# Kernel optimization log

Measured on AMD Instinct MI355X. Metric: run time of the kernel, lower is better.

The kernel has to match this reference:

```python
import jax, jax.numpy as jnp
import numpy as np


def _mlp(x, W0, b0, W1, b1, W2, b2, W3, b3):
    # nlayers=4 MLP: 3->128->128->128->3 with ReLU between layers
    h = jax.nn.relu(x @ W0 + b0)
    h = jax.nn.relu(h @ W1 + b1)
    h = jax.nn.relu(h @ W2 + b2)
    return h @ W3 + b3


def setup_inputs() -> dict:
    key = jax.random.key(0)
    ks = jax.random.split(key, 8)
    B, Nc, Nt, Dx, Dy, H = 8, 1024, 1024, 3, 32, 128
    s = lambda fan: 1.0 / np.sqrt(fan)
    return {
        "xc": jax.random.normal(ks[0], (B, Nc, Dx), jnp.float32),
        "yc": jax.random.normal(ks[1], (B, Nc, Dy), jnp.float32),
        "xt": jax.random.normal(ks[2], (B, Nt, Dx), jnp.float32),
        "W0": jax.random.normal(ks[3], (Dx, H), jnp.float32) * s(Dx),
        "b0": jnp.zeros((H,), jnp.float32),
        "W1": jax.random.normal(ks[4], (H, H), jnp.float32) * s(H),
        "b1": jnp.zeros((H,), jnp.float32),
        "W2": jax.random.normal(ks[5], (H, H), jnp.float32) * s(H),
        "b2": jnp.zeros((H,), jnp.float32),
        "W3": jax.random.normal(ks[6], (H, Dx), jnp.float32) * s(H),
        "b3": jnp.zeros((Dx,), jnp.float32),
    }


def reference(xc, yc, xt, W0, b0, W1, b1, W2, b2, W3, b3):
    # sigmas: per-target, per-coordinate positive scales  (B, Nt, Dx)
    sig = jnp.exp(_mlp(xt, W0, b0, W1, b1, W2, b2, W3, b3))
    # squared differences (B, Nc, Nt, Dx), scaled and reduced over Dx
    A = (xc[:, :, None, :] - xt[:, None, :, :]) ** 2
    P = -(A * sig[:, None, :, :]).sum(axis=3)        # (B, Nc, Nt)
    S = jax.nn.softmax(P, axis=1)                    # softmax over context
    # weighted average of context values: (B, Nt, Dy)
    return jnp.einsum("bnd,bnt->btd", yc, S)
```

## Files before the change

### kernel.cpp

```cpp
#include <hip/hip_runtime.h>
#include <math.h>

#define BB 8
#define NCC 1024
#define NTT 1024
#define HH 128
#define DYY 32
#define NTB 16
#define LOG2E 1.44269504088896340736f

typedef _Float16 half8 __attribute__((ext_vector_type(8)));
typedef float f32x4 __attribute__((ext_vector_type(4)));

#define HB 0
#define RED 2112
#define XCW 2496
#define SIGL 5568
#define SMEM_SZ 5616
#define CMB 0
#define SL 4224
#define HSTRIDE 132

__global__ __launch_bounds__(512, 2) void k_fused(const float* __restrict__ xc,
                                                  const float* __restrict__ yc,
                                                  const float* __restrict__ xt,
                                                  const float* __restrict__ W0,
                                                  const float* __restrict__ b0,
                                                  const float* __restrict__ W1,
                                                  const float* __restrict__ b1,
                                                  const float* __restrict__ W2,
                                                  const float* __restrict__ b2,
                                                  const float* __restrict__ W3,
                                                  const float* __restrict__ b3,
                                                  float* __restrict__ out) {
    const int tid = threadIdx.x;
    const int phys = blockIdx.x;
    const int bid = (phys & 7) * 64 + (phys >> 3);
    const int t0 = bid * NTB;
    const int b = bid >> 6;
    const int wv = tid >> 6;
    const int lane = tid & 63;

    __shared__ float smem[SMEM_SZ];

    const float4* __restrict__ xcG4 = (const float4*)(xc + (size_t)b * NCC * 3);

    const int jg = tid >> 4;
    const int p = tid & 15;
    const int j0 = jg * 4;
    float* hrow = smem + HB + p * HSTRIDE;

    {
        const float* xr = xt + (size_t)(t0 + p) * 3;
        const float x0 = xr[0], x1 = xr[1], x2 = xr[2];
        const float4* W0v = (const float4*)W0;
        const float4 w0a = W0v[jg], w0b = W0v[32 + jg], w0c = W0v[64 + jg];
        const float4 bb0 = ((const float4*)b0)[jg];
        float4 h0;
        h0.x = fmaxf(fmaf(x0, w0a.x, fmaf(x1, w0b.x, fmaf(x2, w0c.x, bb0.x))), 0.f);
        h0.y = fmaxf(fmaf(x0, w0a.y, fmaf(x1, w0b.y, fmaf(x2, w0c.y, bb0.y))), 0.f);
        h0.z = fmaxf(fmaf(x0, w0a.z, fmaf(x1, w0b.z, fmaf(x2, w0c.z, bb0.z))), 0.f);
        h0.w = fmaxf(fmaf(x0, w0a.w, fmaf(x1, w0b.w, fmaf(x2, w0c.w, bb0.w))), 0.f);
        *(float4*)(hrow + j0) = h0;
    }

    {
        float* xcw = smem + XCW + wv * 384;
        if (lane < 48) {
            float4 tx0 = xcG4[wv * 96 + lane];
            float4 tx1 = xcG4[wv * 96 + 48 + lane];
            ((float4*)xcw)[lane] = tx0;
            ((float4*)xcw)[lane + 48] = tx1;
        }
    }
    __syncthreads();

    {
        const int mtl = lane & 15;
        const int mg = lane >> 4;
        const int jcol = wv * 16 + mtl;

#pragma unroll
        for (int l = 0; l < 2; ++l) {
            const float* __restrict__ Wg = (l == 0) ? W1 : W2;
            const float* __restrict__ bi = (l == 0) ? b1 : b2;
            f32x4 dac;
            {
                const float bj = bi[jcol];
                dac[0] = bj; dac[1] = bj; dac[2] = bj; dac[3] = bj;
            }
            float w[8];
#pragma unroll
            for (int i = 0; i < 8; ++i) w[i] = Wg[(mg * 8 + i) * HH + jcol];
#pragma unroll
            for (int c = 0; c < 4; ++c) {
                float wn[8];
                if (c < 3) {
#pragma unroll
                    for (int i = 0; i < 8; ++i)
                        wn[i] = Wg[((c + 1) * 32 + mg * 8 + i) * HH + jcol];
                }
                float hv[8];
                *(float4*)hv =
                    *(const float4*)(smem + HB + mtl * HSTRIDE + c * 32 + mg * 8);
                *(float4*)(hv + 4) =
                    *(const float4*)(smem + HB + mtl * HSTRIDE + c * 32 + mg * 8 + 4);
                half8 a0, a1, bf0, bf1;
#pragma unroll
                for (int i = 0; i < 8; ++i) {
                    const _Float16 ah = (_Float16)hv[i];
                    a0[i] = ah;
                    a1[i] = (_Float16)(hv[i] - (float)ah);
                    const _Float16 wh = (_Float16)w[i];
                    bf0[i] = wh;
                    bf1[i] = (_Float16)(w[i] - (float)wh);
                }
                dac = __builtin_amdgcn_mfma_f32_16x16x32_f16(a0, bf0, dac, 0, 0, 0);
                dac = __builtin_amdgcn_mfma_f32_16x16x32_f16(a0, bf1, dac, 0, 0, 0);
                dac = __builtin_amdgcn_mfma_f32_16x16x32_f16(a1, bf0, dac, 0, 0, 0);
                if (c < 3) {
#pragma unroll
                    for (int i = 0; i < 8; ++i) w[i] = wn[i];
                }
            }
            __syncthreads();
#pragma unroll
            for (int r = 0; r < 4; ++r)
                smem[HB + (mg * 4 + r) * HSTRIDE + jcol] = fmaxf(dac[r], 0.f);
            __syncthreads();
        }
    }

    {
        const float4 o4 = *(const float4*)(hrow + j0);
        const float4* W3v = (const float4*)W3;
        const float4 wr0 = W3v[jg * 3 + 0];
        const float4 wr1 = W3v[jg * 3 + 1];
        const float4 wr2 = W3v[jg * 3 + 2];
        float p0 = o4.x * wr0.x + o4.y * wr0.w + o4.z * wr1.z + o4.w * wr2.y;
        float p1 = o4.x * wr0.y + o4.y * wr1.x + o4.z * wr1.w + o4.w * wr2.z;
        float p2 = o4.x * wr0.z + o4.y * wr1.y + o4.z * wr2.x + o4.w * wr2.w;
        p0 += __shfl_xor(p0, 16, 64);
        p0 += __shfl_xor(p0, 32, 64);
        p1 += __shfl_xor(p1, 16, 64);
        p1 += __shfl_xor(p1, 32, 64);
        p2 += __shfl_xor(p2, 16, 64);
        p2 += __shfl_xor(p2, 32, 64);
        if (lane < 16) {
            smem[RED + wv * 48 + lane * 3 + 0] = p0;
            smem[RED + wv * 48 + lane * 3 + 1] = p1;
            smem[RED + wv * 48 + lane * 3 + 2] = p2;
        }
    }
    __syncthreads();
    if (tid < 48) {
        const int r = tid / 3, cix = tid - r * 3;
        float v = b3[cix];
#pragma unroll
        for (int g2 = 0; g2 < 8; ++g2) v += smem[RED + g2 * 48 + r * 3 + cix];
        smem[SIGL + r * 3 + cix] = __expf(v) * LOG2E;
    }
    __syncthreads();

    const int tl = lane & 15;
    const int g = lane >> 4;

    const float s0 = smem[SIGL + tl * 3 + 0];
    const float s1 = smem[SIGL + tl * 3 + 1];
    const float s2 = smem[SIGL + tl * 3 + 2];
    const float* ar = xt + (size_t)(t0 + tl) * 3;
    const float a0 = ar[0], a1 = ar[1], a2 = ar[2];

    const float* xcw = smem + XCW + wv * 384;
    const float* __restrict__ yB =
        yc + (size_t)b * NCC * DYY + (size_t)(wv * 128 + g * 8) * DYY + tl;

    f32x4 acc0 = {0.f, 0.f, 0.f, 0.f};
    f32x4 acc1 = {0.f, 0.f, 0.f, 0.f};
    float l = 0.f;

#pragma unroll
    for (int c = 0; c < 4; ++c) {
        float by0[8], by1[8];
#pragma unroll
        for (int i = 0; i < 8; ++i) {
            by0[i] = yB[(c * 32 + i) * DYY];
            by1[i] = yB[(c * 32 + i) * DYY + 16];
        }

        float xv[24];
        {
            const float4* xr4 = (const float4*)(xcw + (c * 32 + g * 8) * 3);
#pragma unroll
            for (int q = 0; q < 6; ++q) *(float4*)(xv + q * 4) = xr4[q];
        }
        half8 af, bf0, bf1;
#pragma unroll
        for (int i = 0; i < 8; ++i) {
            const float d0 = xv[i * 3 + 0] - a0;
            const float d1 = xv[i * 3 + 1] - a1;
            const float d2 = xv[i * 3 + 2] - a2;
            const float pp = fmaf(s0, d0 * d0, fmaf(s1, d1 * d1, s2 * (d2 * d2)));
            const _Float16 eh = (_Float16)exp2f(-pp);
            af[i] = eh;
            l += (float)eh;
            bf0[i] = (_Float16)by0[i];
            bf1[i] = (_Float16)by1[i];
        }
        acc0 = __builtin_amdgcn_mfma_f32_16x16x32_f16(af, bf0, acc0, 0, 0, 0);
        acc1 = __builtin_amdgcn_mfma_f32_16x16x32_f16(af, bf1, acc1, 0, 0, 0);
    }

    l += __shfl_xor(l, 16, 64);
    l += __shfl_xor(l, 32, 64);

    __syncthreads();
#pragma unroll
    for (int r = 0; r < 4; ++r) {
        smem[CMB + wv * 528 + (g * 4 + r) * 33 + tl] = acc0[r];
        smem[CMB + wv * 528 + (g * 4 + r) * 33 + 16 + tl] = acc1[r];
    }
    if (lane < 16) smem[SL + wv * 16 + lane] = l;
    __syncthreads();
    {
        const int t = tid >> 5, d = tid & 31;
        float s = 0.f, ls = 0.f;
#pragma unroll
        for (int w = 0; w < 8; ++w) {
            s += smem[CMB + w * 528 + t * 33 + d];
            ls += smem[SL + w * 16 + t];
        }
        out[(size_t)(t0 + t) * DYY + d] = s / ls;
    }
}

extern "C" void kernel_launch(void* const* d_in, const int* in_sizes, int n_in,
                              void* d_out, int out_size, void* d_ws, size_t ws_size,
                              hipStream_t stream) {
    const float* xc = (const float*)d_in[0];
    const float* yc = (const float*)d_in[1];
    const float* xt = (const float*)d_in[2];
    const float* W0 = (const float*)d_in[3];
    const float* b0 = (const float*)d_in[4];
    const float* W1 = (const float*)d_in[5];
    const float* b1 = (const float*)d_in[6];
    const float* W2 = (const float*)d_in[7];
    const float* b2 = (const float*)d_in[8];
    const float* W3 = (const float*)d_in[9];
    const float* b3 = (const float*)d_in[10];
    float* out = (float*)d_out;

    k_fused<<<dim3(BB * NTT / NTB), dim3(512), 0, stream>>>(xc, yc, xt, W0, b0,
                                                            W1, b1, W2, b2, W3,
                                                            b3, out);
}
```

Measured before the change: 85.67 us.

## Double-buffer MLP hidden activations and prefetch weights and yc values

Hidden activations now ping-pong between two shared-memory buffers, which removes one barrier per MLP layer. W1 is loaded before the first barrier and W2 before the layer-1 barrier so global loads overlap with synchronisation. The yc loads in the attention loop are software-pipelined one chunk ahead. Shared memory grows to about 31KB and register pressure rises, which may affect the 2-blocks-per-CU occupancy.

Measured after the change: 85.02 us. No clear change (-0.8%).

```diff
diff --git a/kernel.cpp b/kernel.cpp
--- a/kernel.cpp
+++ b/kernel.cpp
@@ -12,11 +12,12 @@
 typedef _Float16 half8 __attribute__((ext_vector_type(8)));
 typedef float f32x4 __attribute__((ext_vector_type(4)));
 
-#define HB 0
-#define RED 2112
-#define XCW 2496
-#define SIGL 5568
-#define SMEM_SZ 5616
+#define HB0 0
+#define HB1 2112
+#define RED 4224
+#define XCW 4608
+#define SIGL 7680
+#define SMEM_SZ 7728
 #define CMB 0
 #define SL 4224
 #define HSTRIDE 132
@@ -48,7 +49,6 @@
     const int jg = tid >> 4;
     const int p = tid & 15;
     const int j0 = jg * 4;
-    float* hrow = smem + HB + p * HSTRIDE;
 
     {
         const float* xr = xt + (size_t)(t0 + p) * 3;
@@ -61,7 +61,7 @@
         h0.y = fmaxf(fmaf(x0, w0a.y, fmaf(x1, w0b.y, fmaf(x2, w0c.y, bb0.y))), 0.f);
         h0.z = fmaxf(fmaf(x0, w0a.z, fmaf(x1, w0b.z, fmaf(x2, w0c.z, bb0.z))), 0.f);
         h0.w = fmaxf(fmaf(x0, w0a.w, fmaf(x1, w0b.w, fmaf(x2, w0c.w, bb0.w))), 0.f);
-        *(float4*)(hrow + j0) = h0;
+        *(float4*)(smem + HB0 + p * HSTRIDE + j0) = h0;
     }
 
     {
@@ -73,13 +73,19 @@
             ((float4*)xcw)[lane + 48] = tx1;
         }
     }
-    __syncthreads();
 
     {
         const int mtl = lane & 15;
         const int mg = lane >> 4;
         const int jcol = wv * 16 + mtl;
 
+        float w[8];
+#pragma unroll
+        for (int i = 0; i < 8; ++i) w[i] = W1[(mg * 8 + i) * HH + jcol];
+        __syncthreads();
+
+        float* hsrc = smem + HB0;
+        float* hdst = smem + HB1;
 #pragma unroll
         for (int l = 0; l < 2; ++l) {
             const float* __restrict__ Wg = (l == 0) ? W1 : W2;
@@ -89,9 +95,6 @@
                 const float bj = bi[jcol];
                 dac[0] = bj; dac[1] = bj; dac[2] = bj; dac[3] = bj;
             }
-            float w[8];
-#pragma unroll
-            for (int i = 0; i < 8; ++i) w[i] = Wg[(mg * 8 + i) * HH + jcol];
 #pragma unroll
             for (int c = 0; c < 4; ++c) {
                 float wn[8];
@@ -102,9 +105,9 @@
                 }
                 float hv[8];
                 *(float4*)hv =
-                    *(const float4*)(smem + HB + mtl * HSTRIDE + c * 32 + mg * 8);
+                    *(const float4*)(hsrc + mtl * HSTRIDE + c * 32 + mg * 8);
                 *(float4*)(hv + 4) =
-                    *(const float4*)(smem + HB + mtl * HSTRIDE + c * 32 + mg * 8 + 4);
+                    *(const float4*)(hsrc + mtl * HSTRIDE + c * 32 + mg * 8 + 4);
                 half8 a0, a1, bf0, bf1;
 #pragma unroll
                 for (int i = 0; i < 8; ++i) {
@@ -123,16 +126,20 @@
                     for (int i = 0; i < 8; ++i) w[i] = wn[i];
                 }
             }
+#pragma unroll
+            for (int r = 0; r < 4; ++r)
+                hdst[(mg * 4 + r) * HSTRIDE + jcol] = fmaxf(dac[r], 0.f);
+            if (l == 0) {
+#pragma unroll
+                for (int i = 0; i < 8; ++i) w[i] = W2[(mg * 8 + i) * HH + jcol];
+            }
             __syncthreads();
-#pragma unroll
-            for (int r = 0; r < 4; ++r)
-                smem[HB + (mg * 4 + r) * HSTRIDE + jcol] = fmaxf(dac[r], 0.f);
-            __syncthreads();
-        }
-    }
-
-    {
-        const float4 o4 = *(const float4*)(hrow + j0);
+            float* tmp = hsrc; hsrc = hdst; hdst = tmp;
+        }
+    }
+
+    {
+        const float4 o4 = *(const float4*)(smem + HB0 + p * HSTRIDE + j0);
         const float4* W3v = (const float4*)W3;
         const float4 wr0 = W3v[jg * 3 + 0];
         const float4 wr1 = W3v[jg * 3 + 1];
@@ -179,13 +186,22 @@
     f32x4 acc1 = {0.f, 0.f, 0.f, 0.f};
     float l = 0.f;
 
+    float by0[8], by1[8];
+#pragma unroll
+    for (int i = 0; i < 8; ++i) {
+        by0[i] = yB[i * DYY];
+        by1[i] = yB[i * DYY + 16];
+    }
+
 #pragma unroll
     for (int c = 0; c < 4; ++c) {
-        float by0[8], by1[8];
-#pragma unroll
-        for (int i = 0; i < 8; ++i) {
-            by0[i] = yB[(c * 32 + i) * DYY];
-            by1[i] = yB[(c * 32 + i) * DYY + 16];
+        float bn0[8], bn1[8];
+        if (c < 3) {
+#pragma unroll
+            for (int i = 0; i < 8; ++i) {
+                bn0[i] = yB[((c + 1) * 32 + i) * DYY];
+                bn1[i] = yB[((c + 1) * 32 + i) * DYY + 16];
+            }
         }
 
         float xv[24];
@@ -209,6 +225,11 @@
         }
         acc0 = __builtin_amdgcn_mfma_f32_16x16x32_f16(af, bf0, acc0, 0, 0, 0);
         acc1 = __builtin_amdgcn_mfma_f32_16x16x32_f16(af, bf1, acc1, 0, 0, 0);
+
+        if (c < 3) {
+#pragma unroll
+            for (int i = 0; i < 8; ++i) { by0[i] = bn0[i]; by1[i] = bn1[i]; }
+        }
     }
 
     l += __shfl_xor(l, 16, 64);
```
